# Kernel tuning notes

Hardware: AMD Instinct MI355X
Metric: run time of the kernel (lower is better)

Reference implementation:

```python
import jax, jax.numpy as jnp
import numpy as np

N, E, IN_CH, OUT_CH = 8192, 4096, 256, 256
EPS = 1e-06


def setup_inputs() -> dict:
    key = jax.random.key(0)
    k1, k2, k3, k4 = jax.random.split(key, 4)
    x = jax.random.normal(k1, (N, IN_CH), dtype=jnp.float32)
    H = jax.random.uniform(k2, (N, E), dtype=jnp.float32)
    # nn.Linear(in_ch, out_ch): weight [out_ch, in_ch], bias [out_ch]
    lim = 1.0 / np.sqrt(IN_CH)
    W = jax.random.uniform(k3, (OUT_CH, IN_CH), dtype=jnp.float32, minval=-lim, maxval=lim)
    b = jax.random.uniform(k4, (OUT_CH,), dtype=jnp.float32, minval=-lim, maxval=lim)
    return {"x": x, "H": H, "W": W, "b": b}


def reference(x, H, W, b):
    # A = Dv^{-1/2} H De^{-1} H^T Dv^{-1/2}; out = (A x) W^T + b
    d_e = H.sum(axis=0)                      # [E] hyperedge degrees
    d_v = H.sum(axis=1)                      # [N] node degrees
    de_inv = 1.0 / (d_e + EPS)               # [E]
    dv_is = (d_v + EPS) ** -0.5              # [N]
    # Diagonal matmuls expressed as row/col scaling (same math, no NxN/ExE diag GEMMs)
    xs = dv_is[:, None] * x                  # Dv^{-1/2} x            [N, C]
    t = de_inv[:, None] * (H.T @ xs)         # De^{-1} H^T (...)      [E, C]
    out = dv_is[:, None] * (H @ t)           # Dv^{-1/2} H (...)      [N, C]
    return out @ W.T + b
```

## Files before the change

### kernel.cpp

```cpp
#include <hip/hip_runtime.h>

#define NNODE 8192
#define NEDGE 4096
#define NCH   256
#define EPSV  1e-6f

typedef float  f32x4  __attribute__((ext_vector_type(4)));
typedef short  bf16x8 __attribute__((ext_vector_type(8)));
typedef unsigned short u16;
typedef unsigned int   u32;

static __device__ __forceinline__ u16 f2bf(float f) {
  union { float f; u32 u; } c; c.f = f;
  return (u16)((c.u + 0x7FFFu + ((c.u >> 16) & 1u)) >> 16);
}

static __device__ __forceinline__ void gload16(const u16* g, u16* l) {
  __builtin_amdgcn_global_load_lds((const __attribute__((address_space(1))) void*)g,
                                   (__attribute__((address_space(3))) void*)l,
                                   16, 0, 0);
}

__global__ __launch_bounds__(256) void prep_h(const float* __restrict__ H,
                                              u16* __restrict__ Hb,
                                              u16* __restrict__ HbT,
                                              float* __restrict__ d_v,
                                              float* __restrict__ d_e) {
  __shared__ uint2 Tp[64][17];
  __shared__ float csp[16][68];
  __shared__ float rsum[64];
  const int t = threadIdx.x, a = t >> 4, b = t & 15;
  const int r0 = blockIdx.x * 64, c0 = blockIdx.y * 64;

  float4 v[4];
  #pragma unroll
  for (int i = 0; i < 4; ++i)
    v[i] = *(const float4*)&H[(size_t)(r0 + 4 * a + i) * NEDGE + c0 + 4 * b];

  #pragma unroll
  for (int i = 0; i < 4; ++i) {
    float rp = v[i].x + v[i].y + v[i].z + v[i].w;
    rp += __shfl_xor(rp, 1); rp += __shfl_xor(rp, 2);
    rp += __shfl_xor(rp, 4); rp += __shfl_xor(rp, 8);
    if (b == 0) rsum[4 * a + i] = rp;
  }
  csp[a][4 * b + 0] = v[0].x + v[1].x + v[2].x + v[3].x;
  csp[a][4 * b + 1] = v[0].y + v[1].y + v[2].y + v[3].y;
  csp[a][4 * b + 2] = v[0].z + v[1].z + v[2].z + v[3].z;
  csp[a][4 * b + 3] = v[0].w + v[1].w + v[2].w + v[3].w;

  u16 e[4][4];
  #pragma unroll
  for (int i = 0; i < 4; ++i) {
    e[i][0] = f2bf(v[i].x); e[i][1] = f2bf(v[i].y);
    e[i][2] = f2bf(v[i].z); e[i][3] = f2bf(v[i].w);
  }
  #pragma unroll
  for (int i = 0; i < 4; ++i) {
    uint2 hv;
    hv.x = (u32)e[i][0] | ((u32)e[i][1] << 16);
    hv.y = (u32)e[i][2] | ((u32)e[i][3] << 16);
    *(uint2*)&Hb[(size_t)(r0 + 4 * a + i) * NEDGE + c0 + 4 * b] = hv;
  }
  #pragma unroll
  for (int j = 0; j < 4; ++j) {
    uint2 tv;
    tv.x = (u32)e[0][j] | ((u32)e[1][j] << 16);
    tv.y = (u32)e[2][j] | ((u32)e[3][j] << 16);
    Tp[4 * b + j][a] = tv;
  }
  __syncthreads();

  #pragma unroll
  for (int s = 0; s < 2; ++s) {
    const int idx = t + 256 * s;
    const int c = idx >> 3, g = idx & 7;
    const uint2 p0 = Tp[c][2 * g], p1 = Tp[c][2 * g + 1];
    uint4 w; w.x = p0.x; w.y = p0.y; w.z = p1.x; w.w = p1.y;
    *(uint4*)&HbT[(size_t)(c0 + c) * NNODE + r0 + 8 * g] = w;
  }
  if (t < 64) {
    float s = 0.f;
    #pragma unroll
    for (int r = 0; r < 16; ++r) s += csp[r][t];
    atomicAdd(&d_e[c0 + t], s);
    atomicAdd(&d_v[r0 + t], rsum[t]);
  }
}

__global__ __launch_bounds__(256) void prep_x(const float* __restrict__ x,
                                              const float* __restrict__ d_v,
                                              u16* __restrict__ xsT) {
  __shared__ uint2 Tp[64][17];
  const int t = threadIdx.x, a = t >> 4, b = t & 15;
  const int r0 = blockIdx.x * 64, c0 = blockIdx.y * 64;

  u16 e[4][4];
  #pragma unroll
  for (int i = 0; i < 4; ++i) {
    const int n = r0 + 4 * a + i;
    const float s = rsqrtf(d_v[n] + EPSV);
    const float4 v = *(const float4*)&x[(size_t)n * NCH + c0 + 4 * b];
    e[i][0] = f2bf(v.x * s); e[i][1] = f2bf(v.y * s);
    e[i][2] = f2bf(v.z * s); e[i][3] = f2bf(v.w * s);
  }
  #pragma unroll
  for (int j = 0; j < 4; ++j) {
    uint2 tv;
    tv.x = (u32)e[0][j] | ((u32)e[1][j] << 16);
    tv.y = (u32)e[2][j] | ((u32)e[3][j] << 16);
    Tp[4 * b + j][a] = tv;
  }
  __syncthreads();
  #pragma unroll
  for (int s = 0; s < 2; ++s) {
    const int idx = t + 256 * s;
    const int c = idx >> 3, g = idx & 7;
    const uint2 p0 = Tp[c][2 * g], p1 = Tp[c][2 * g + 1];
    uint4 w; w.x = p0.x; w.y = p0.y; w.z = p1.x; w.w = p1.y;
    *(uint4*)&xsT[(size_t)(c0 + c) * NNODE + r0 + 8 * g] = w;
  }
}

__global__ __launch_bounds__(256) void prep_w(const float* __restrict__ W,
                                              u16* __restrict__ Wb) {
  const int i = (blockIdx.x * 256 + threadIdx.x) * 8;
  const float4 a = *(const float4*)&W[i];
  const float4 b = *(const float4*)&W[i + 4];
  uint4 v;
  v.x = (u32)f2bf(a.x) | ((u32)f2bf(a.y) << 16);
  v.y = (u32)f2bf(a.z) | ((u32)f2bf(a.w) << 16);
  v.z = (u32)f2bf(b.x) | ((u32)f2bf(b.y) << 16);
  v.w = (u32)f2bf(b.z) | ((u32)f2bf(b.w) << 16);
  *(uint4*)&Wb[i] = v;
}

__global__ __launch_bounds__(256) void init_out(const float* __restrict__ b,
                                                float* __restrict__ out) {
  const int i = (blockIdx.x * 256 + threadIdx.x) * 4;
  const float4 bb = *(const float4*)&b[i & 255];
  *(float4*)&out[i] = bb;
}

template <int ROWS, int NT>
static __device__ __forceinline__ void stage_gl(const u16* __restrict__ base,
                                                int row0, int K, int kt,
                                                u16* lds, int tid) {
  const int w = tid >> 6, l = tid & 63;
  #pragma unroll
  for (int i = 0; i < (ROWS * 8) / NT; ++i) {
    const int slot = i * NT + w * 64 + l;
    const int row = slot >> 3, ch = slot & 7;
    const int sch = ch ^ (row & 7);
    gload16(base + (size_t)(row0 + row) * K + kt + sch * 8,
            lds + (size_t)(i * NT + w * 64) * 8);
  }
}

template <int ROWS, int NT>
static __device__ __forceinline__ void stage_f32(const float* __restrict__ base,
                                                 int row0, int K, int kt,
                                                 const float* __restrict__ sv,
                                                 u16* lds, int tid) {
  for (int idx = tid; idx < ROWS * 8; idx += NT) {
    const int row = idx >> 3, ch = idx & 7;
    const float s = 1.0f / (sv[row0 + row] + EPSV);
    const size_t g = (size_t)(row0 + row) * K + kt + ch * 8;
    const float4 v0 = *(const float4*)&base[g];
    const float4 v1 = *(const float4*)&base[g + 4];
    uint4 pv;
    pv.x = (u32)f2bf(v0.x * s) | ((u32)f2bf(v0.y * s) << 16);
    pv.y = (u32)f2bf(v0.z * s) | ((u32)f2bf(v0.w * s) << 16);
    pv.z = (u32)f2bf(v1.x * s) | ((u32)f2bf(v1.y * s) << 16);
    pv.w = (u32)f2bf(v1.z * s) | ((u32)f2bf(v1.w * s) << 16);
    *(uint4*)&lds[row * 64 + ((ch ^ (row & 7)) * 8)] = pv;
  }
}

template <int BM, int BN, int WM, int WN, int BSRC, int EPI>
__global__ __launch_bounds__(WM * WN * 64) void gemm_nt(
    const u16* __restrict__ Aptr, const void* __restrict__ Bptr,
    int K, int KC,
    const float* __restrict__ svb, const float* __restrict__ sve,
    void* __restrict__ Cout, int ldc) {
  constexpr int BK = 64;
  constexpr int NT = WM * WN * 64;
  constexpr int WMR = BM / WM, WNR = BN / WN;
  constexpr int FM = WMR / 16, FN = WNR / 16;
  __shared__ u16 lds_a[BM * BK];
  __shared__ u16 lds_b[BN * BK];

  const int tid  = threadIdx.x;
  const int lane = tid & 63;
  const int w    = tid >> 6;
  const int wm   = w / WN, wn = w % WN;

  const int nx = gridDim.x, ny = gridDim.y;
  const int nwg = nx * ny * gridDim.z;
  int lid = blockIdx.x + nx * (blockIdx.y + ny * blockIdx.z);
  if ((nwg & 7) == 0) lid = (lid & 7) * (nwg >> 3) + (lid >> 3);
  const int bx = lid % nx;
  const int byz = lid / nx;
  const int by = byz % ny, bz = byz / ny;

  const int m0 = bx * BM;
  const int n0 = by * BN;
  const int k0 = bz * KC;

  f32x4 acc[FM][FN];
  #pragma unroll
  for (int fm = 0; fm < FM; ++fm)
    #pragma unroll
    for (int fn = 0; fn < FN; ++fn)
      acc[fm][fn] = (f32x4){0.f, 0.f, 0.f, 0.f};

  for (int kt = k0; kt < k0 + KC; kt += BK) {
    __syncthreads();
    stage_gl<BM, NT>(Aptr, m0, K, kt, lds_a, tid);
    if constexpr (BSRC == 0) {
      stage_gl<BN, NT>((const u16*)Bptr, n0, K, kt, lds_b, tid);
    } else {
      stage_f32<BN, NT>((const float*)Bptr, n0, K, kt, svb, lds_b, tid);
    }
    __syncthreads();

    #pragma unroll
    for (int kk = 0; kk < 2; ++kk) {
      bf16x8 af[FM], bfv[FN];
      #pragma unroll
      for (int fm = 0; fm < FM; ++fm) {
        const int row = wm * WMR + fm * 16 + (lane & 15);
        const int ch  = kk * 4 + (lane >> 4);
        af[fm] = *(const bf16x8*)&lds_a[row * BK + ((ch ^ (row & 7)) * 8)];
      }
      #pragma unroll
      for (int fn = 0; fn < FN; ++fn) {
        const int row = wn * WNR + fn * 16 + (lane & 15);
        const int ch  = kk * 4 + (lane >> 4);
        bfv[fn] = *(const bf16x8*)&lds_b[row * BK + ((ch ^ (row & 7)) * 8)];
      }
      #pragma unroll
      for (int fm = 0; fm < FM; ++fm)
        #pragma unroll
        for (int fn = 0; fn < FN; ++fn)
          acc[fm][fn] = __builtin_amdgcn_mfma_f32_16x16x32_bf16(
              af[fm], bfv[fn], acc[fm][fn], 0, 0, 0);
    }
  }

  if constexpr (EPI == 0) {
    float* C = (float*)Cout;
    #pragma unroll
    for (int fm = 0; fm < FM; ++fm) {
      const int rowb = m0 + wm * WMR + fm * 16 + ((lane >> 4) << 2);
      #pragma unroll
      for (int fn = 0; fn < FN; ++fn) {
        const int col = n0 + wn * WNR + fn * 16 + (lane & 15);
        #pragma unroll
        for (int r = 0; r < 4; ++r)
          atomicAdd(&C[(size_t)(rowb + r) * ldc + col], acc[fm][fn][r]);
      }
    }
  } else if constexpr (EPI == 1) {
    float* C = (float*)Cout;
    #pragma unroll
    for (int fm = 0; fm < FM; ++fm) {
      const int rowb = m0 + wm * WMR + fm * 16 + ((lane >> 4) << 2);
      float s[4];
      #pragma unroll
      for (int r = 0; r < 4; ++r) s[r] = rsqrtf(sve[rowb + r] + EPSV);
      #pragma unroll
      for (int fn = 0; fn < FN; ++fn) {
        const int col = n0 + wn * WNR + fn * 16 + (lane & 15);
        #pragma unroll
        for (int r = 0; r < 4; ++r)
          atomicAdd(&C[(size_t)(rowb + r) * ldc + col], acc[fm][fn][r] * s[r]);
      }
    }
  } else {
    u16* C = (u16*)Cout;
    #pragma unroll
    for (int fm = 0; fm < FM; ++fm) {
      const int rowb = m0 + wm * WMR + fm * 16 + ((lane >> 4) << 2);
      #pragma unroll
      for (int fn = 0; fn < FN; ++fn) {
        const int col = n0 + wn * WNR + fn * 16 + (lane & 15);
        #pragma unroll
        for (int r = 0; r < 4; ++r)
          C[(size_t)(rowb + r) * ldc + col] = f2bf(acc[fm][fn][r]);
      }
    }
  }
}

extern "C" void kernel_launch(void* const* d_in, const int* in_sizes, int n_in,
                              void* d_out, int out_size, void* d_ws, size_t ws_size,
                              hipStream_t stream) {
  const float* x = (const float*)d_in[0];
  const float* H = (const float*)d_in[1];
  const float* W = (const float*)d_in[2];
  const float* b = (const float*)d_in[3];
  float* out = (float*)d_out;

  char* ws = (char*)d_ws;
  u16*   HbT  = (u16*)(ws);
  u16*   Hb   = (u16*)(ws + 67108864ull);
  u16*   xsT  = (u16*)(ws + 134217728ull);
  float* tAcc = (float*)(ws + 138412032ull);
  u16*   uT   = (u16*)(ws + 142606336ull);
  u16*   Wb   = (u16*)(ws + 144703488ull);
  float* dv   = (float*)(ws + 144834560ull);
  float* de   = (float*)(ws + 144867328ull);

  hipMemsetAsync(dv, 0, (NNODE + NEDGE) * sizeof(float), stream);
  hipMemsetAsync(tAcc, 0, (size_t)NEDGE * NCH * sizeof(float), stream);

  prep_h<<<dim3(NNODE / 64, NEDGE / 64), 256, 0, stream>>>(H, Hb, HbT, dv, de);
  prep_x<<<dim3(NNODE / 64, NCH / 64), 256, 0, stream>>>(x, dv, xsT);
  prep_w<<<32, 256, 0, stream>>>(W, Wb);
  init_out<<<(NNODE * NCH) / 1024, 256, 0, stream>>>(b, out);

  gemm_nt<128, 128, 2, 2, 0, 0><<<dim3(NEDGE / 128, NCH / 128, 16), 256, 0, stream>>>(
      HbT, xsT, NNODE, NNODE / 16, nullptr, nullptr, tAcc, NCH);
  gemm_nt<64, 128, 2, 2, 1, 2><<<dim3(4, NEDGE / 128, 1), 256, 0, stream>>>(
      Wb, tAcc, NCH, NCH, de, nullptr, uT, NEDGE);
  gemm_nt<128, 128, 2, 2, 0, 1><<<dim3(NNODE / 128, NCH / 128, 8), 256, 0, stream>>>(
      Hb, uT, NEDGE, NEDGE / 8, nullptr, dv, out, NCH);
}
```

Baseline: 389.8 us.

## Drop bf16 H copy and stream fp32 H directly into the final GEMM

The prep kernel no longer writes a row-major bf16 copy of H; only the transposed bf16 copy is kept. The last GEMM gains an fp32 A-source path that loads H and converts it to bf16 while staging tiles into LDS. This is meant to remove one full-size write of H and its later read-back. Both large GEMMs also widen to 256-column tiles with 512 threads, so each H tile is read once instead of twice. The diff also drops the XCD-aware block remapping, adds an occupancy hint to launch_bounds, and does the prep transposes in fp32 in LDS. The risk is that the fp32 staging path uses ordinary synchronous loads rather than async global-to-LDS copies, and it moves twice as many bytes per element.

```diff
diff --git a/kernel.cpp b/kernel.cpp
--- a/kernel.cpp
+++ b/kernel.cpp
@@ -21,12 +21,20 @@
                                    16, 0, 0);
 }
 
+static __device__ __forceinline__ uint4 pack8(const float4& a, const float4& c) {
+  uint4 v;
+  v.x = (u32)f2bf(a.x) | ((u32)f2bf(a.y) << 16);
+  v.y = (u32)f2bf(a.z) | ((u32)f2bf(a.w) << 16);
+  v.z = (u32)f2bf(c.x) | ((u32)f2bf(c.y) << 16);
+  v.w = (u32)f2bf(c.z) | ((u32)f2bf(c.w) << 16);
+  return v;
+}
+
 __global__ __launch_bounds__(256) void prep_h(const float* __restrict__ H,
-                                              u16* __restrict__ Hb,
                                               u16* __restrict__ HbT,
                                               float* __restrict__ d_v,
                                               float* __restrict__ d_e) {
-  __shared__ uint2 Tp[64][17];
+  __shared__ float T[64][68];
   __shared__ float csp[16][68];
   __shared__ float rsum[64];
   const int t = threadIdx.x, a = t >> 4, b = t & 15;
@@ -49,25 +57,15 @@
   csp[a][4 * b + 2] = v[0].z + v[1].z + v[2].z + v[3].z;
   csp[a][4 * b + 3] = v[0].w + v[1].w + v[2].w + v[3].w;
 
-  u16 e[4][4];
-  #pragma unroll
-  for (int i = 0; i < 4; ++i) {
-    e[i][0] = f2bf(v[i].x); e[i][1] = f2bf(v[i].y);
-    e[i][2] = f2bf(v[i].z); e[i][3] = f2bf(v[i].w);
-  }
-  #pragma unroll
-  for (int i = 0; i < 4; ++i) {
-    uint2 hv;
-    hv.x = (u32)e[i][0] | ((u32)e[i][1] << 16);
-    hv.y = (u32)e[i][2] | ((u32)e[i][3] << 16);
-    *(uint2*)&Hb[(size_t)(r0 + 4 * a + i) * NEDGE + c0 + 4 * b] = hv;
-  }
-  #pragma unroll
-  for (int j = 0; j < 4; ++j) {
-    uint2 tv;
-    tv.x = (u32)e[0][j] | ((u32)e[1][j] << 16);
-    tv.y = (u32)e[2][j] | ((u32)e[3][j] << 16);
-    Tp[4 * b + j][a] = tv;
+  {
+    float4 w0 = {v[0].x, v[1].x, v[2].x, v[3].x};
+    float4 w1 = {v[0].y, v[1].y, v[2].y, v[3].y};
+    float4 w2 = {v[0].z, v[1].z, v[2].z, v[3].z};
+    float4 w3 = {v[0].w, v[1].w, v[2].w, v[3].w};
+    *(float4*)&T[4 * b + 0][4 * a] = w0;
+    *(float4*)&T[4 * b + 1][4 * a] = w1;
+    *(float4*)&T[4 * b + 2][4 * a] = w2;
+    *(float4*)&T[4 * b + 3][4 * a] = w3;
   }
   __syncthreads();
 
@@ -75,9 +73,9 @@
   for (int s = 0; s < 2; ++s) {
     const int idx = t + 256 * s;
     const int c = idx >> 3, g = idx & 7;
-    const uint2 p0 = Tp[c][2 * g], p1 = Tp[c][2 * g + 1];
-    uint4 w; w.x = p0.x; w.y = p0.y; w.z = p1.x; w.w = p1.y;
-    *(uint4*)&HbT[(size_t)(c0 + c) * NNODE + r0 + 8 * g] = w;
+    const float4 p0 = *(const float4*)&T[c][8 * g];
+    const float4 p1 = *(const float4*)&T[c][8 * g + 4];
+    *(uint4*)&HbT[(size_t)(c0 + c) * NNODE + r0 + 8 * g] = pack8(p0, p1);
   }
   if (t < 64) {
     float s = 0.f;
@@ -91,34 +89,37 @@
 __global__ __launch_bounds__(256) void prep_x(const float* __restrict__ x,
                                               const float* __restrict__ d_v,
                                               u16* __restrict__ xsT) {
-  __shared__ uint2 Tp[64][17];
+  __shared__ float T[64][68];
   const int t = threadIdx.x, a = t >> 4, b = t & 15;
   const int r0 = blockIdx.x * 64, c0 = blockIdx.y * 64;
 
-  u16 e[4][4];
+  float4 v[4];
   #pragma unroll
   for (int i = 0; i < 4; ++i) {
     const int n = r0 + 4 * a + i;
     const float s = rsqrtf(d_v[n] + EPSV);
-    const float4 v = *(const float4*)&x[(size_t)n * NCH + c0 + 4 * b];
-    e[i][0] = f2bf(v.x * s); e[i][1] = f2bf(v.y * s);
-    e[i][2] = f2bf(v.z * s); e[i][3] = f2bf(v.w * s);
-  }
-  #pragma unroll
-  for (int j = 0; j < 4; ++j) {
-    uint2 tv;
-    tv.x = (u32)e[0][j] | ((u32)e[1][j] << 16);
-    tv.y = (u32)e[2][j] | ((u32)e[3][j] << 16);
-    Tp[4 * b + j][a] = tv;
+    float4 w = *(const float4*)&x[(size_t)n * NCH + c0 + 4 * b];
+    w.x *= s; w.y *= s; w.z *= s; w.w *= s;
+    v[i] = w;
+  }
+  {
+    float4 w0 = {v[0].x, v[1].x, v[2].x, v[3].x};
+    float4 w1 = {v[0].y, v[1].y, v[2].y, v[3].y};
+    float4 w2 = {v[0].z, v[1].z, v[2].z, v[3].z};
+    float4 w3 = {v[0].w, v[1].w, v[2].w, v[3].w};
+    *(float4*)&T[4 * b + 0][4 * a] = w0;
+    *(float4*)&T[4 * b + 1][4 * a] = w1;
+    *(float4*)&T[4 * b + 2][4 * a] = w2;
+    *(float4*)&T[4 * b + 3][4 * a] = w3;
   }
   __syncthreads();
   #pragma unroll
   for (int s = 0; s < 2; ++s) {
     const int idx = t + 256 * s;
     const int c = idx >> 3, g = idx & 7;
-    const uint2 p0 = Tp[c][2 * g], p1 = Tp[c][2 * g + 1];
-    uint4 w; w.x = p0.x; w.y = p0.y; w.z = p1.x; w.w = p1.y;
-    *(uint4*)&xsT[(size_t)(c0 + c) * NNODE + r0 + 8 * g] = w;
+    const float4 p0 = *(const float4*)&T[c][8 * g];
+    const float4 p1 = *(const float4*)&T[c][8 * g + 4];
+    *(uint4*)&xsT[(size_t)(c0 + c) * NNODE + r0 + 8 * g] = pack8(p0, p1);
   }
 }
 
@@ -127,12 +128,7 @@
   const int i = (blockIdx.x * 256 + threadIdx.x) * 8;
   const float4 a = *(const float4*)&W[i];
   const float4 b = *(const float4*)&W[i + 4];
-  uint4 v;
-  v.x = (u32)f2bf(a.x) | ((u32)f2bf(a.y) << 16);
-  v.y = (u32)f2bf(a.z) | ((u32)f2bf(a.w) << 16);
-  v.z = (u32)f2bf(b.x) | ((u32)f2bf(b.y) << 16);
-  v.w = (u32)f2bf(b.z) | ((u32)f2bf(b.w) << 16);
-  *(uint4*)&Wb[i] = v;
+  *(uint4*)&Wb[i] = pack8(a, b);
 }
 
 __global__ __launch_bounds__(256) void init_out(const float* __restrict__ b,
@@ -157,29 +153,27 @@
   }
 }
 
-template <int ROWS, int NT>
+template <int ROWS, int NT, int SCALE>
 static __device__ __forceinline__ void stage_f32(const float* __restrict__ base,
                                                  int row0, int K, int kt,
                                                  const float* __restrict__ sv,
                                                  u16* lds, int tid) {
   for (int idx = tid; idx < ROWS * 8; idx += NT) {
     const int row = idx >> 3, ch = idx & 7;
-    const float s = 1.0f / (sv[row0 + row] + EPSV);
+    float s = 1.0f;
+    if constexpr (SCALE == 1) s = 1.0f / (sv[row0 + row] + EPSV);
     const size_t g = (size_t)(row0 + row) * K + kt + ch * 8;
-    const float4 v0 = *(const float4*)&base[g];
-    const float4 v1 = *(const float4*)&base[g + 4];
-    uint4 pv;
-    pv.x = (u32)f2bf(v0.x * s) | ((u32)f2bf(v0.y * s) << 16);
-    pv.y = (u32)f2bf(v0.z * s) | ((u32)f2bf(v0.w * s) << 16);
-    pv.z = (u32)f2bf(v1.x * s) | ((u32)f2bf(v1.y * s) << 16);
-    pv.w = (u32)f2bf(v1.z * s) | ((u32)f2bf(v1.w * s) << 16);
-    *(uint4*)&lds[row * 64 + ((ch ^ (row & 7)) * 8)] = pv;
-  }
-}
-
-template <int BM, int BN, int WM, int WN, int BSRC, int EPI>
-__global__ __launch_bounds__(WM * WN * 64) void gemm_nt(
-    const u16* __restrict__ Aptr, const void* __restrict__ Bptr,
+    float4 v0 = *(const float4*)&base[g];
+    float4 v1 = *(const float4*)&base[g + 4];
+    v0.x *= s; v0.y *= s; v0.z *= s; v0.w *= s;
+    v1.x *= s; v1.y *= s; v1.z *= s; v1.w *= s;
+    *(uint4*)&lds[row * 64 + ((ch ^ (row & 7)) * 8)] = pack8(v0, v1);
+  }
+}
+
+template <int BM, int BN, int WM, int WN, int ASRC, int BSRC, int EPI>
+__global__ __launch_bounds__(WM * WN * 64, 4) void gemm_nt(
+    const void* __restrict__ Aptr, const void* __restrict__ Bptr,
     int K, int KC,
     const float* __restrict__ svb, const float* __restrict__ sve,
     void* __restrict__ Cout, int ldc) {
@@ -194,18 +188,9 @@
   const int lane = tid & 63;
   const int w    = tid >> 6;
   const int wm   = w / WN, wn = w % WN;
-
-  const int nx = gridDim.x, ny = gridDim.y;
-  const int nwg = nx * ny * gridDim.z;
-  int lid = blockIdx.x + nx * (blockIdx.y + ny * blockIdx.z);
-  if ((nwg & 7) == 0) lid = (lid & 7) * (nwg >> 3) + (lid >> 3);
-  const int bx = lid % nx;
-  const int byz = lid / nx;
-  const int by = byz % ny, bz = byz / ny;
-
-  const int m0 = bx * BM;
-  const int n0 = by * BN;
-  const int k0 = bz * KC;
+  const int m0   = blockIdx.x * BM;
+  const int n0   = blockIdx.y * BN;
+  const int k0   = blockIdx.z * KC;
 
   f32x4 acc[FM][FN];
   #pragma unroll
@@ -216,11 +201,15 @@
 
   for (int kt = k0; kt < k0 + KC; kt += BK) {
     __syncthreads();
-    stage_gl<BM, NT>(Aptr, m0, K, kt, lds_a, tid);
+    if constexpr (ASRC == 0) {
+      stage_gl<BM, NT>((const u16*)Aptr, m0, K, kt, lds_a, tid);
+    } else {
+      stage_f32<BM, NT, 0>((const float*)Aptr, m0, K, kt, nullptr, lds_a, tid);
+    }
     if constexpr (BSRC == 0) {
       stage_gl<BN, NT>((const u16*)Bptr, n0, K, kt, lds_b, tid);
     } else {
-      stage_f32<BN, NT>((const float*)Bptr, n0, K, kt, svb, lds_b, tid);
+      stage_f32<BN, NT, 1>((const float*)Bptr, n0, K, kt, svb, lds_b, tid);
     }
     __syncthreads();
 
@@ -304,26 +293,25 @@
 
   char* ws = (char*)d_ws;
   u16*   HbT  = (u16*)(ws);
-  u16*   Hb   = (u16*)(ws + 67108864ull);
-  u16*   xsT  = (u16*)(ws + 134217728ull);
-  float* tAcc = (float*)(ws + 138412032ull);
-  u16*   uT   = (u16*)(ws + 142606336ull);
-  u16*   Wb   = (u16*)(ws + 144703488ull);
-  float* dv   = (float*)(ws + 144834560ull);
-  float* de   = (float*)(ws + 144867328ull);
+  u16*   xsT  = (u16*)(ws + 67108864ull);
+  float* tAcc = (float*)(ws + 71303168ull);
+  u16*   uT   = (u16*)(ws + 75497472ull);
+  u16*   Wb   = (u16*)(ws + 77594624ull);
+  float* dv   = (float*)(ws + 77725696ull);
+  float* de   = (float*)(ws + 77758464ull);
 
   hipMemsetAsync(dv, 0, (NNODE + NEDGE) * sizeof(float), stream);
   hipMemsetAsync(tAcc, 0, (size_t)NEDGE * NCH * sizeof(float), stream);
 
-  prep_h<<<dim3(NNODE / 64, NEDGE / 64), 256, 0, stream>>>(H, Hb, HbT, dv, de);
+  prep_h<<<dim3(NNODE / 64, NEDGE / 64), 256, 0, stream>>>(H, HbT, dv, de);
   prep_x<<<dim3(NNODE / 64, NCH / 64), 256, 0, stream>>>(x, dv, xsT);
   prep_w<<<32, 256, 0, stream>>>(W, Wb);
   init_out<<<(NNODE * NCH) / 1024, 256, 0, stream>>>(b, out);
 
-  gemm_nt<128, 128, 2, 2, 0, 0><<<dim3(NEDGE / 128, NCH / 128, 16), 256, 0, stream>>>(
+  gemm_nt<128, 256, 2, 4, 0, 0, 0><<<dim3(NEDGE / 128, 1, 16), 512, 0, stream>>>(
       HbT, xsT, NNODE, NNODE / 16, nullptr, nullptr, tAcc, NCH);
-  gemm_nt<64, 128, 2, 2, 1, 2><<<dim3(4, NEDGE / 128, 1), 256, 0, stream>>>(
+  gemm_nt<64, 64, 2, 2, 0, 1, 2><<<dim3(4, NEDGE / 64, 1), 256, 0, stream>>>(
       Wb, tAcc, NCH, NCH, de, nullptr, uT, NEDGE);
-  gemm_nt<128, 128, 2, 2, 0, 1><<<dim3(NNODE / 128, NCH / 128, 8), 256, 0, stream>>>(
-      Hb, uT, NEDGE, NEDGE / 8, nullptr, dv, out, NCH);
-}
+  gemm_nt<128, 256, 2, 4, 1, 0, 1><<<dim3(NNODE / 128, 1, 8), 512, 0, stream>>>(
+      H, uT, NEDGE, NEDGE / 8, nullptr, dv, out, NCH);
+}
```

Result: faster. 379.2 us (-2.7%).
